# Optimization experiments

Hardware: AMD Instinct MI355X
Metric: run time of the kernel (lower is better)

The kernel has to match this reference:

```python
import jax, jax.numpy as jnp
import numpy as np

NUM_NODES = 256
IN_FEAT = 64
HIDDEN = 512
N_CLASSES = 2
BATCH = 256


def setup_inputs() -> dict:
    key = jax.random.key(0)
    ks = jax.random.split(key, 10)
    return {
        "z": jax.random.normal(ks[0], (BATCH, 1, NUM_NODES, NUM_NODES), dtype=jnp.float32),
        "node_emb": jax.random.normal(ks[1], (NUM_NODES, IN_FEAT), dtype=jnp.float32),
        "w1": jax.random.normal(ks[2], (IN_FEAT, HIDDEN), dtype=jnp.float32) * (1.0 / np.sqrt(IN_FEAT)),
        "b1": jnp.zeros((HIDDEN,), dtype=jnp.float32),
        "w2": jax.random.normal(ks[3], (HIDDEN, HIDDEN), dtype=jnp.float32) * (1.0 / np.sqrt(HIDDEN)),
        "b2": jnp.zeros((HIDDEN,), dtype=jnp.float32),
        "w3": jax.random.normal(ks[4], (HIDDEN, HIDDEN), dtype=jnp.float32) * (1.0 / np.sqrt(HIDDEN)),
        "b3": jnp.zeros((HIDDEN,), dtype=jnp.float32),
        "fcw": jax.random.normal(ks[5], (HIDDEN, N_CLASSES), dtype=jnp.float32) * (1.0 / np.sqrt(HIDDEN)),
        "fcb": jnp.zeros((N_CLASSES,), dtype=jnp.float32),
    }


def reference(z, node_emb, w1, b1, w2, b2, w3, b3, fcw, fcb):
    # z: (B, 1, N, N) latent interpreted as weighted adjacency
    z_sq = jnp.squeeze(z, axis=1)                         # (B, N, N)
    A = jax.nn.sigmoid(z_sq)
    A = (A + jnp.swapaxes(A, 1, 2)) * 0.5                  # symmetrize
    A_hat = A + jnp.eye(A.shape[-1], dtype=A.dtype)[None]  # add self loops
    D_hat = jnp.sum(A_hat, axis=2) + 1e-6                  # (B, N) degrees
    d_inv_sqrt = D_hat ** -0.5
    # norm_A = D^{-1/2} A_hat D^{-1/2} via row/col scaling (same math as diag bmm)
    norm_A = A_hat * d_inv_sqrt[:, :, None] * d_inv_sqrt[:, None, :]

    X = jnp.broadcast_to(node_emb[None], (z.shape[0],) + node_emb.shape)  # (B, N, F)
    H1 = jax.nn.relu(jnp.einsum('bij,bjh->bih', norm_A, X @ w1 + b1))
    H2 = jax.nn.relu(jnp.einsum('bij,bjh->bih', norm_A, H1 @ w2 + b2))
    H3 = jax.nn.relu(jnp.einsum('bij,bjh->bih', norm_A, H2 @ w3 + b3))
    graph_emb = jnp.mean(H3, axis=1)                       # (B, H)
    logits = graph_emb @ fcw + fcb                         # (B, n_classes)
    return logits
```

## Files before the change

### kernel.cpp

```cpp
#include <hip/hip_runtime.h>
#include <stdint.h>

#define B_ 256
#define N_ 256
#define F_ 64
#define H_ 512

typedef _Float16 f16;
typedef _Float16 f16x8 __attribute__((ext_vector_type(8)));
typedef _Float16 f16x4 __attribute__((ext_vector_type(4)));
typedef float    f32x4 __attribute__((ext_vector_type(4)));

__device__ __forceinline__ float sigmoidf_(float x) {
    return 1.0f / (1.0f + __expf(-x));
}

__global__ __launch_bounds__(256) void k_sums(const float* __restrict__ z,
                                              f16* __restrict__ S,
                                              float* __restrict__ R,
                                              float* __restrict__ Cpart) {
    int b = blockIdx.y, c = blockIdx.x;
    int tid = threadIdx.x, lane = tid & 63, w = tid >> 6;
    float colacc[4] = {0.f, 0.f, 0.f, 0.f};
    for (int r = 0; r < 16; r++) {
        int i = c * 64 + w * 16 + r;
        size_t base = ((size_t)(b * N_ + i)) * N_;
        float4 v = *(const float4*)(z + base + lane * 4);
        float s0 = sigmoidf_(v.x), s1 = sigmoidf_(v.y),
              s2 = sigmoidf_(v.z), s3 = sigmoidf_(v.w);
        f16x4 sv = { (f16)s0, (f16)s1, (f16)s2, (f16)s3 };
        *(f16x4*)(S + base + lane * 4) = sv;
        colacc[0] += s0; colacc[1] += s1; colacc[2] += s2; colacc[3] += s3;
        float rs = s0 + s1 + s2 + s3;
        for (int off = 32; off; off >>= 1) rs += __shfl_down(rs, off, 64);
        if (lane == 0) R[b * N_ + i] = rs;
    }
    __shared__ float cbuf[4][N_];
    #pragma unroll
    for (int k = 0; k < 4; k++) cbuf[w][lane * 4 + k] = colacc[k];
    __syncthreads();
    float s4 = cbuf[0][tid] + cbuf[1][tid] + cbuf[2][tid] + cbuf[3][tid];
    Cpart[((size_t)c * B_ + b) * N_ + tid] = s4;
}

__global__ __launch_bounds__(256) void k_norma3(const f16* __restrict__ S,
                                                const float* __restrict__ R,
                                                const float* __restrict__ Cpart,
                                                f16* __restrict__ nA) {
    __shared__ f16 T0[128 * 129];
    __shared__ f16 T1[128 * 129];
    __shared__ float Dv[N_];
    int b = blockIdx.y, t = blockIdx.x;
    int tid = threadIdx.x;
    const f16* Sb = S + (size_t)b * N_ * N_;
    f16* Ab = nA + (size_t)b * N_ * N_;

    float cs = Cpart[(size_t)b * N_ + tid]
             + Cpart[((size_t)B_ + b) * N_ + tid]
             + Cpart[((size_t)2 * B_ + b) * N_ + tid]
             + Cpart[((size_t)3 * B_ + b) * N_ + tid];
    Dv[tid] = rsqrtf(1.0f + 1e-6f + 0.5f * (R[b * N_ + tid] + cs));

    auto stage = [&](const f16* src, f16* dst) {
        #pragma unroll
        for (int it = 0; it < 8; it++) {
            int u = it * 256 + tid;
            int r = u >> 4, c8 = (u & 15) * 8;
            *(f16x8*)&dst[r * 129 + c8] = *(const f16x8*)&src[(size_t)r * N_ + c8];
        }
    };
    if (t == 0)      stage(Sb, T0);
    else if (t == 1) stage(Sb + 128 * N_ + 128, T0);
    else           { stage(Sb + 128, T0); stage(Sb + (size_t)128 * N_, T1); }
    __syncthreads();

    auto emit = [&](const f16* Dir, const f16* Mir, int i0, int j0) {
        #pragma unroll
        for (int it = 0; it < 8; it++) {
            int il = it * 16 + (tid >> 4), jl8 = (tid & 15) * 8;
            float di = Dv[i0 + il];
            f16x8 d = *(const f16x8*)&Dir[il * 129 + jl8];
            f16x8 o;
            #pragma unroll
            for (int k = 0; k < 8; k++) {
                float v = 0.5f * ((float)d[k] + (float)Mir[(jl8 + k) * 129 + il]);
                if (i0 + il == j0 + jl8 + k) v += 1.0f;
                o[k] = (f16)(v * di * Dv[j0 + jl8 + k]);
            }
            *(f16x8*)&Ab[(size_t)(i0 + il) * N_ + j0 + jl8] = o;
        }
    };
    if (t == 0)      emit(T0, T0, 0, 0);
    else if (t == 1) emit(T0, T0, 128, 128);
    else           { emit(T0, T1, 0, 128); emit(T1, T0, 128, 0); }
}

__global__ __launch_bounds__(256) void k_prep(const float* __restrict__ ne,
                                              const float* __restrict__ w1,
                                              const float* __restrict__ b1,
                                              const float* __restrict__ w2,
                                              const float* __restrict__ w3,
                                              f16* __restrict__ XW1t,
                                              f16* __restrict__ w2t,
                                              f16* __restrict__ w3t) {
    int bid = blockIdx.x;
    if (bid < 512) {
        int h = bid, node = threadIdx.x;
        float s = b1[h];
        #pragma unroll 8
        for (int k = 0; k < F_; k++) s += ne[node * F_ + k] * w1[k * H_ + h];
        XW1t[h * N_ + node] = (f16)s;
    } else {
        int idx4 = bid - 512;
        int which = idx4 >> 10;
        const float* src = which ? w3 : w2;
        f16* dst = which ? w3t : w2t;
        int idx = (idx4 & 1023) * 256 + threadIdx.x;
        int k = idx >> 9, n = idx & 511;
        dst[n * H_ + k] = (f16)src[k * H_ + n];
    }
}

template <int KDIM, int MODE>
__global__ __launch_bounds__(256, 4) void k_gemm(const f16* __restrict__ A, long aBatch,
                                                 const f16* __restrict__ Bt, long bBatch,
                                                 f16* __restrict__ Out,
                                                 const float* __restrict__ bias,
                                                 float* __restrict__ gp) {
    __shared__ f16 As[128 * 64];
    __shared__ f16 Bs[128 * 64];
    const int tid  = threadIdx.x;
    const int lane = tid & 63, wave = tid >> 6;
    const int wm = wave >> 1, wn = wave & 1;

    const int lin = blockIdx.x;
    const int xcd = lin & 7, q = lin >> 3;
    const int n_t = q & 3, p = q >> 2;
    const int grp = xcd * 64 + p;
    const int b   = grp >> 1, m_t = grp & 1;
    const int m0 = m_t * 128, n0 = n_t * 128;

    const f16* Ab = A + (size_t)b * aBatch;
    const f16* Bb = Bt + (size_t)b * bBatch;

    f32x4 acc[4][4];
    #pragma unroll
    for (int i = 0; i < 4; i++)
        #pragma unroll
        for (int j = 0; j < 4; j++)
            #pragma unroll
            for (int r = 0; r < 4; r++) acc[i][j][r] = 0.0f;

    const int lr = lane >> 3;
    const int kc = (lane & 7) ^ lr;

    const int ln15 = lane & 15;

    for (int kk = 0; kk < KDIM; kk += 64) {
        #pragma unroll
        for (int c = 0; c < 4; c++) {
            int chunk = wave * 4 + c;
            int row = chunk * 8 + lr;
            __builtin_amdgcn_global_load_lds(
                (__attribute__((address_space(1))) void*)(Ab + (size_t)(m0 + row) * KDIM + kk + kc * 8),
                (__attribute__((address_space(3))) void*)(&As[chunk * 512]), 16, 0, 0);
            __builtin_amdgcn_global_load_lds(
                (__attribute__((address_space(1))) void*)(Bb + (size_t)(n0 + row) * KDIM + kk + kc * 8),
                (__attribute__((address_space(3))) void*)(&Bs[chunk * 512]), 16, 0, 0);
        }
        __syncthreads();

        #pragma unroll
        for (int ks = 0; ks < 2; ks++) {
            const int rkc = ks * 4 + (lane >> 4);
            f16x8 aF[4];
            #pragma unroll
            for (int t = 0; t < 4; t++) {
                int ra = wm * 64 + t * 16 + ln15;
                aF[t] = *(const f16x8*)&As[(ra * 8 + (rkc ^ (ra & 7))) * 8];
            }
            #pragma unroll
            for (int h2 = 0; h2 < 2; h2++) {
                f16x8 bF[2];
                #pragma unroll
                for (int t = 0; t < 2; t++) {
                    int rb = wn * 64 + (h2 * 2 + t) * 16 + ln15;
                    bF[t] = *(const f16x8*)&Bs[(rb * 8 + (rkc ^ (rb & 7))) * 8];
                }
                #pragma unroll
                for (int mt = 0; mt < 4; mt++)
                    #pragma unroll
                    for (int t = 0; t < 2; t++)
                        acc[mt][h2 * 2 + t] = __builtin_amdgcn_mfma_f32_16x16x32_f16(aF[mt], bF[t], acc[mt][h2 * 2 + t], 0, 0, 0);
            }
        }
        __syncthreads();
    }

    const int quad = lane >> 4;
    if (MODE == 0) {
        f16* Ob = Out + (size_t)b * (N_ * H_);
        #pragma unroll
        for (int mt = 0; mt < 4; mt++) {
            int node = m0 + wm * 64 + mt * 16 + quad * 4;
            #pragma unroll
            for (int nt = 0; nt < 4; nt++) {
                int h = n0 + wn * 64 + nt * 16 + ln15;
                #pragma unroll
                for (int rr = 0; rr < 4; rr++) {
                    float v = acc[mt][nt][rr];
                    v = v > 0.f ? v : 0.f;
                    Ob[(size_t)(node + rr) * H_ + h] = (f16)v;
                }
            }
        }
    } else if (MODE == 1) {
        f16* Ob = Out + (size_t)b * (H_ * N_);
        #pragma unroll
        for (int nt = 0; nt < 4; nt++) {
            int n = n0 + wn * 64 + nt * 16 + ln15;
            float bv = bias[n];
            #pragma unroll
            for (int mt = 0; mt < 4; mt++) {
                int node = m0 + wm * 64 + mt * 16 + quad * 4;
                f16x4 v;
                #pragma unroll
                for (int rr = 0; rr < 4; rr++) v[rr] = (f16)(acc[mt][nt][rr] + bv);
                *(f16x4*)&Ob[(size_t)n * N_ + node] = v;
            }
        }
    } else {
        float part[4];
        #pragma unroll
        for (int nt = 0; nt < 4; nt++) {
            float partial = 0.f;
            #pragma unroll
            for (int mt = 0; mt < 4; mt++)
                #pragma unroll
                for (int rr = 0; rr < 4; rr++) {
                    float v = acc[mt][nt][rr];
                    partial += (v > 0.f ? v : 0.f);
                }
            partial += __shfl_down(partial, 32, 64);
            partial += __shfl_down(partial, 16, 64);
            part[nt] = partial;
        }
        __syncthreads();
        float* red = (float*)&As[0];
        if (quad == 0) {
            #pragma unroll
            for (int nt = 0; nt < 4; nt++)
                red[wave * 64 + nt * 16 + ln15] = part[nt];
        }
        __syncthreads();
        if (tid < 128) {
            int wnl = tid >> 6, hl = tid & 63;
            float v = red[wnl * 64 + hl] + red[(wnl + 2) * 64 + hl];
            gp[((size_t)m_t * B_ + b) * H_ + n0 + wnl * 64 + hl] = v;
        }
    }
}

__global__ __launch_bounds__(256) void k_logits(const float* __restrict__ gp,
                                                const float* __restrict__ fcw,
                                                const float* __restrict__ fcb,
                                                float* __restrict__ out) {
    int b = blockIdx.x, tid = threadIdx.x;
    const float* g0p = gp + (size_t)b * H_;
    const float* g1p = gp + (size_t)(B_ + b) * H_;
    float g0 = g0p[tid] + g1p[tid];
    float g1 = g0p[tid + 256] + g1p[tid + 256];
    float p0 = g0 * fcw[tid * 2 + 0] + g1 * fcw[(tid + 256) * 2 + 0];
    float p1 = g0 * fcw[tid * 2 + 1] + g1 * fcw[(tid + 256) * 2 + 1];
    for (int off = 32; off; off >>= 1) {
        p0 += __shfl_down(p0, off, 64);
        p1 += __shfl_down(p1, off, 64);
    }
    __shared__ float r0[4], r1[4];
    int lane = tid & 63, w = tid >> 6;
    if (lane == 0) { r0[w] = p0; r1[w] = p1; }
    __syncthreads();
    const float inv = 1.0f / N_;
    if (tid == 0) out[b * 2 + 0] = (r0[0] + r0[1] + r0[2] + r0[3]) * inv + fcb[0];
    if (tid == 1) out[b * 2 + 1] = (r1[0] + r1[1] + r1[2] + r1[3]) * inv + fcb[1];
}

extern "C" void kernel_launch(void* const* d_in, const int* in_sizes, int n_in,
                              void* d_out, int out_size, void* d_ws, size_t ws_size,
                              hipStream_t stream) {
    const float* z   = (const float*)d_in[0];
    const float* ne  = (const float*)d_in[1];
    const float* w1  = (const float*)d_in[2];
    const float* b1  = (const float*)d_in[3];
    const float* w2  = (const float*)d_in[4];
    const float* b2  = (const float*)d_in[5];
    const float* w3  = (const float*)d_in[6];
    const float* b3  = (const float*)d_in[7];
    const float* fcw = (const float*)d_in[8];
    const float* fcb = (const float*)d_in[9];
    float* out = (float*)d_out;

    char* ws = (char*)d_ws;
    f16*   T     = (f16*)(ws + 0);
    float* R     = (float*)(ws + 0);
    float* Cpart = (float*)(ws + 262144);
    f16*   nA    = (f16*)(ws + 67108864);
    f16*   Hh    = (f16*)(ws + 100663296);
    f16*   S     = (f16*)(ws + 100663296);
    float* gpart = (float*)(ws + 100663296);
    f16*   XW1t  = (f16*)(ws + 167772160);
    f16*   w2t   = (f16*)(ws + 168034304);
    f16*   w3t   = (f16*)(ws + 168558592);

    k_sums  <<<dim3(4, B_), 256, 0, stream>>>(z, S, R, Cpart);
    k_norma3<<<dim3(3, B_), 256, 0, stream>>>(S, R, Cpart, nA);
    k_prep  <<<2560,        256, 0, stream>>>(ne, w1, b1, w2, w3, XW1t, w2t, w3t);

    k_gemm<256, 0><<<2048, 256, 0, stream>>>(nA, 65536, XW1t, 0, Hh, nullptr, nullptr);
    k_gemm<512, 1><<<2048, 256, 0, stream>>>(Hh, 131072, w2t, 0, T, b2, nullptr);
    k_gemm<256, 0><<<2048, 256, 0, stream>>>(nA, 65536, T, 131072, Hh, nullptr, nullptr);
    k_gemm<512, 1><<<2048, 256, 0, stream>>>(Hh, 131072, w3t, 0, T, b3, nullptr);
    k_gemm<256, 2><<<2048, 256, 0, stream>>>(nA, 65536, T, 131072, nullptr, nullptr, gpart);

    k_logits<<<B_, 256, 0, stream>>>(gpart, fcw, fcb, out);
}
```

Measured before the change: 332.1 us.

## Load GEMM MFMA fragments directly from global memory and merge prep kernels

The batched GEMM no longer stages A and B tiles through LDS. Each wave now loads its MFMA fragments straight from global memory into registers, double-buffered with a ping-pong register scheme, which removes the LDS round trips and block-wide barriers. Launch bounds drop to 3 blocks per SM to make room for the extra registers. The sigmoid/sum kernel and the weight-prep kernel are merged into one launch to save a kernel launch. The risk is that each wave now fetches overlapping rows without LDS sharing, which raises global and L2 traffic, and that the lower occupancy hides latency less well.

After: 596.8 us. 1.8x slower.

```diff
diff --git a/kernel.cpp b/kernel.cpp
--- a/kernel.cpp
+++ b/kernel.cpp
@@ -15,32 +15,58 @@
     return 1.0f / (1.0f + __expf(-x));
 }
 
-__global__ __launch_bounds__(256) void k_sums(const float* __restrict__ z,
-                                              f16* __restrict__ S,
-                                              float* __restrict__ R,
-                                              float* __restrict__ Cpart) {
-    int b = blockIdx.y, c = blockIdx.x;
-    int tid = threadIdx.x, lane = tid & 63, w = tid >> 6;
-    float colacc[4] = {0.f, 0.f, 0.f, 0.f};
-    for (int r = 0; r < 16; r++) {
-        int i = c * 64 + w * 16 + r;
-        size_t base = ((size_t)(b * N_ + i)) * N_;
-        float4 v = *(const float4*)(z + base + lane * 4);
-        float s0 = sigmoidf_(v.x), s1 = sigmoidf_(v.y),
-              s2 = sigmoidf_(v.z), s3 = sigmoidf_(v.w);
-        f16x4 sv = { (f16)s0, (f16)s1, (f16)s2, (f16)s3 };
-        *(f16x4*)(S + base + lane * 4) = sv;
-        colacc[0] += s0; colacc[1] += s1; colacc[2] += s2; colacc[3] += s3;
-        float rs = s0 + s1 + s2 + s3;
-        for (int off = 32; off; off >>= 1) rs += __shfl_down(rs, off, 64);
-        if (lane == 0) R[b * N_ + i] = rs;
+__global__ __launch_bounds__(256) void k_pre(const float* __restrict__ z,
+                                             const float* __restrict__ ne,
+                                             const float* __restrict__ w1,
+                                             const float* __restrict__ b1,
+                                             const float* __restrict__ w2,
+                                             const float* __restrict__ w3,
+                                             f16* __restrict__ S,
+                                             float* __restrict__ R,
+                                             float* __restrict__ Cpart,
+                                             f16* __restrict__ XW1t,
+                                             f16* __restrict__ w2t,
+                                             f16* __restrict__ w3t) {
+    int bid = blockIdx.x;
+    int tid = threadIdx.x;
+    if (bid < 1024) {
+        int b = bid >> 2, c = bid & 3;
+        int lane = tid & 63, w = tid >> 6;
+        float colacc[4] = {0.f, 0.f, 0.f, 0.f};
+        for (int r = 0; r < 16; r++) {
+            int i = c * 64 + w * 16 + r;
+            size_t base = ((size_t)(b * N_ + i)) * N_;
+            float4 v = *(const float4*)(z + base + lane * 4);
+            float s0 = sigmoidf_(v.x), s1 = sigmoidf_(v.y),
+                  s2 = sigmoidf_(v.z), s3 = sigmoidf_(v.w);
+            f16x4 sv = { (f16)s0, (f16)s1, (f16)s2, (f16)s3 };
+            *(f16x4*)(S + base + lane * 4) = sv;
+            colacc[0] += s0; colacc[1] += s1; colacc[2] += s2; colacc[3] += s3;
+            float rs = s0 + s1 + s2 + s3;
+            for (int off = 32; off; off >>= 1) rs += __shfl_down(rs, off, 64);
+            if (lane == 0) R[b * N_ + i] = rs;
+        }
+        __shared__ float cbuf[4][N_];
+        #pragma unroll
+        for (int k = 0; k < 4; k++) cbuf[w][lane * 4 + k] = colacc[k];
+        __syncthreads();
+        float s4 = cbuf[0][tid] + cbuf[1][tid] + cbuf[2][tid] + cbuf[3][tid];
+        Cpart[((size_t)c * B_ + b) * N_ + tid] = s4;
+    } else if (bid < 1536) {
+        int h = bid - 1024, node = tid;
+        float s = b1[h];
+        #pragma unroll 8
+        for (int k = 0; k < F_; k++) s += ne[node * F_ + k] * w1[k * H_ + h];
+        XW1t[h * N_ + node] = (f16)s;
+    } else {
+        int idx4 = bid - 1536;
+        int which = idx4 >> 10;
+        const float* src = which ? w3 : w2;
+        f16* dst = which ? w3t : w2t;
+        int idx = (idx4 & 1023) * 256 + tid;
+        int k = idx >> 9, n = idx & 511;
+        dst[n * H_ + k] = (f16)src[k * H_ + n];
     }
-    __shared__ float cbuf[4][N_];
-    #pragma unroll
-    for (int k = 0; k < 4; k++) cbuf[w][lane * 4 + k] = colacc[k];
-    __syncthreads();
-    float s4 = cbuf[0][tid] + cbuf[1][tid] + cbuf[2][tid] + cbuf[3][tid];
-    Cpart[((size_t)c * B_ + b) * N_ + tid] = s4;
 }
 
 __global__ __launch_bounds__(256) void k_norma3(const f16* __restrict__ S,
@@ -95,43 +121,17 @@
     else           { emit(T0, T1, 0, 128); emit(T1, T0, 128, 0); }
 }
 
-__global__ __launch_bounds__(256) void k_prep(const float* __restrict__ ne,
-                                              const float* __restrict__ w1,
-                                              const float* __restrict__ b1,
-                                              const float* __restrict__ w2,
-                                              const float* __restrict__ w3,
-                                              f16* __restrict__ XW1t,
-                                              f16* __restrict__ w2t,
-                                              f16* __restrict__ w3t) {
-    int bid = blockIdx.x;
-    if (bid < 512) {
-        int h = bid, node = threadIdx.x;
-        float s = b1[h];
-        #pragma unroll 8
-        for (int k = 0; k < F_; k++) s += ne[node * F_ + k] * w1[k * H_ + h];
-        XW1t[h * N_ + node] = (f16)s;
-    } else {
-        int idx4 = bid - 512;
-        int which = idx4 >> 10;
-        const float* src = which ? w3 : w2;
-        f16* dst = which ? w3t : w2t;
-        int idx = (idx4 & 1023) * 256 + threadIdx.x;
-        int k = idx >> 9, n = idx & 511;
-        dst[n * H_ + k] = (f16)src[k * H_ + n];
-    }
-}
-
 template <int KDIM, int MODE>
-__global__ __launch_bounds__(256, 4) void k_gemm(const f16* __restrict__ A, long aBatch,
+__global__ __launch_bounds__(256, 3) void k_gemm(const f16* __restrict__ A, long aBatch,
                                                  const f16* __restrict__ Bt, long bBatch,
                                                  f16* __restrict__ Out,
                                                  const float* __restrict__ bias,
                                                  float* __restrict__ gp) {
-    __shared__ f16 As[128 * 64];
-    __shared__ f16 Bs[128 * 64];
+    __shared__ float red[256];
     const int tid  = threadIdx.x;
     const int lane = tid & 63, wave = tid >> 6;
     const int wm = wave >> 1, wn = wave & 1;
+    const int ln15 = lane & 15, rkc = lane >> 4;
 
     const int lin = blockIdx.x;
     const int xcd = lin & 7, q = lin >> 3;
@@ -140,9 +140,6 @@
     const int b   = grp >> 1, m_t = grp & 1;
     const int m0 = m_t * 128, n0 = n_t * 128;
 
-    const f16* Ab = A + (size_t)b * aBatch;
-    const f16* Bb = Bt + (size_t)b * bBatch;
-
     f32x4 acc[4][4];
     #pragma unroll
     for (int i = 0; i < 4; i++)
@@ -151,53 +148,37 @@
             #pragma unroll
             for (int r = 0; r < 4; r++) acc[i][j][r] = 0.0f;
 
-    const int lr = lane >> 3;
-    const int kc = (lane & 7) ^ lr;
-
-    const int ln15 = lane & 15;
-
-    for (int kk = 0; kk < KDIM; kk += 64) {
-        #pragma unroll
-        for (int c = 0; c < 4; c++) {
-            int chunk = wave * 4 + c;
-            int row = chunk * 8 + lr;
-            __builtin_amdgcn_global_load_lds(
-                (__attribute__((address_space(1))) void*)(Ab + (size_t)(m0 + row) * KDIM + kk + kc * 8),
-                (__attribute__((address_space(3))) void*)(&As[chunk * 512]), 16, 0, 0);
-            __builtin_amdgcn_global_load_lds(
-                (__attribute__((address_space(1))) void*)(Bb + (size_t)(n0 + row) * KDIM + kk + kc * 8),
-                (__attribute__((address_space(3))) void*)(&Bs[chunk * 512]), 16, 0, 0);
-        }
-        __syncthreads();
-
-        #pragma unroll
-        for (int ks = 0; ks < 2; ks++) {
-            const int rkc = ks * 4 + (lane >> 4);
-            f16x8 aF[4];
-            #pragma unroll
-            for (int t = 0; t < 4; t++) {
-                int ra = wm * 64 + t * 16 + ln15;
-                aF[t] = *(const f16x8*)&As[(ra * 8 + (rkc ^ (ra & 7))) * 8];
-            }
-            #pragma unroll
-            for (int h2 = 0; h2 < 2; h2++) {
-                f16x8 bF[2];
-                #pragma unroll
-                for (int t = 0; t < 2; t++) {
-                    int rb = wn * 64 + (h2 * 2 + t) * 16 + ln15;
-                    bF[t] = *(const f16x8*)&Bs[(rb * 8 + (rkc ^ (rb & 7))) * 8];
-                }
-                #pragma unroll
-                for (int mt = 0; mt < 4; mt++)
-                    #pragma unroll
-                    for (int t = 0; t < 2; t++)
-                        acc[mt][h2 * 2 + t] = __builtin_amdgcn_mfma_f32_16x16x32_f16(aF[mt], bF[t], acc[mt][h2 * 2 + t], 0, 0, 0);
-            }
-        }
-        __syncthreads();
+    const f16* pA = A  + (size_t)b * aBatch + (size_t)(m0 + wm * 64 + ln15) * KDIM + rkc * 8;
+    const f16* pB = Bt + (size_t)b * bBatch + (size_t)(n0 + wn * 64 + ln15) * KDIM + rkc * 8;
+
+    f16x8 aC[4], bC[4], aN[4], bN[4];
+
+    auto load4 = [&](f16x8* af, f16x8* bf, int s) {
+        #pragma unroll
+        for (int t = 0; t < 4; t++) {
+            af[t] = *(const f16x8*)(pA + (size_t)t * 16 * KDIM + s * 32);
+            bf[t] = *(const f16x8*)(pB + (size_t)t * 16 * KDIM + s * 32);
+        }
+    };
+    auto domfma = [&](const f16x8* af, const f16x8* bf) {
+        #pragma unroll
+        for (int mt = 0; mt < 4; mt++)
+            #pragma unroll
+            for (int nt = 0; nt < 4; nt++)
+                acc[mt][nt] = __builtin_amdgcn_mfma_f32_16x16x32_f16(af[mt], bf[nt], acc[mt][nt], 0, 0, 0);
+    };
+
+    constexpr int NS = KDIM / 32;
+    load4(aC, bC, 0);
+    #pragma unroll 1
+    for (int s = 0; s < NS; s += 2) {
+        load4(aN, bN, s + 1);
+        domfma(aC, bC);
+        if (s + 2 < NS) load4(aC, bC, s + 2);
+        domfma(aN, bN);
     }
 
-    const int quad = lane >> 4;
+    const int quad = rkc;
     if (MODE == 0) {
         f16* Ob = Out + (size_t)b * (N_ * H_);
         #pragma unroll
@@ -245,8 +226,6 @@
             partial += __shfl_down(partial, 16, 64);
             part[nt] = partial;
         }
-        __syncthreads();
-        float* red = (float*)&As[0];
         if (quad == 0) {
             #pragma unroll
             for (int nt = 0; nt < 4; nt++)
@@ -312,9 +291,8 @@
     f16*   w2t   = (f16*)(ws + 168034304);
     f16*   w3t   = (f16*)(ws + 168558592);
 
-    k_sums  <<<dim3(4, B_), 256, 0, stream>>>(z, S, R, Cpart);
+    k_pre   <<<3584,        256, 0, stream>>>(z, ne, w1, b1, w2, w3, S, R, Cpart, XW1t, w2t, w3t);
     k_norma3<<<dim3(3, B_), 256, 0, stream>>>(S, R, Cpart, nA);
-    k_prep  <<<2560,        256, 0, stream>>>(ne, w1, b1, w2, w3, XW1t, w2t, w3t);
 
     k_gemm<256, 0><<<2048, 256, 0, stream>>>(nA, 65536, XW1t, 0, Hh, nullptr, nullptr);
     k_gemm<512, 1><<<2048, 256, 0, stream>>>(Hh, 131072, w2t, 0, T, b2, nullptr);
```

## Merge sigmoid-sum and weight prep kernels, split rows finer, rotate GEMM K-order

Applied to the files above, without the earlier changes.

The sigmoid/row-column sum kernel and the weight preparation kernel become one launch with 4608 blocks. Each sum block now covers 32 rows instead of 64, so there are 8 column partials, and the normalisation kernel sums all 8. The GEMM K-loop start is rotated per block so concurrent blocks read different K slices, which is meant to spread memory and cache traffic. The cost is one fewer launch and more parallelism in the sum stage, in exchange for more partial-sum traffic and a less predictable access order.

New measurement: 335.4 us. No clear change (+1.0%).

```diff
diff --git a/kernel.cpp b/kernel.cpp
--- a/kernel.cpp
+++ b/kernel.cpp
@@ -15,32 +15,58 @@
     return 1.0f / (1.0f + __expf(-x));
 }
 
-__global__ __launch_bounds__(256) void k_sums(const float* __restrict__ z,
-                                              f16* __restrict__ S,
-                                              float* __restrict__ R,
-                                              float* __restrict__ Cpart) {
-    int b = blockIdx.y, c = blockIdx.x;
-    int tid = threadIdx.x, lane = tid & 63, w = tid >> 6;
-    float colacc[4] = {0.f, 0.f, 0.f, 0.f};
-    for (int r = 0; r < 16; r++) {
-        int i = c * 64 + w * 16 + r;
-        size_t base = ((size_t)(b * N_ + i)) * N_;
-        float4 v = *(const float4*)(z + base + lane * 4);
-        float s0 = sigmoidf_(v.x), s1 = sigmoidf_(v.y),
-              s2 = sigmoidf_(v.z), s3 = sigmoidf_(v.w);
-        f16x4 sv = { (f16)s0, (f16)s1, (f16)s2, (f16)s3 };
-        *(f16x4*)(S + base + lane * 4) = sv;
-        colacc[0] += s0; colacc[1] += s1; colacc[2] += s2; colacc[3] += s3;
-        float rs = s0 + s1 + s2 + s3;
-        for (int off = 32; off; off >>= 1) rs += __shfl_down(rs, off, 64);
-        if (lane == 0) R[b * N_ + i] = rs;
+__global__ __launch_bounds__(256) void k_pre(const float* __restrict__ z,
+                                             const float* __restrict__ ne,
+                                             const float* __restrict__ w1,
+                                             const float* __restrict__ b1,
+                                             const float* __restrict__ w2,
+                                             const float* __restrict__ w3,
+                                             f16* __restrict__ S,
+                                             float* __restrict__ R,
+                                             float* __restrict__ Cpart,
+                                             f16* __restrict__ XW1t,
+                                             f16* __restrict__ w2t,
+                                             f16* __restrict__ w3t) {
+    int bid = blockIdx.x;
+    int tid = threadIdx.x;
+    if (bid < 2048) {
+        int b = bid >> 3, c = bid & 7;
+        int lane = tid & 63, w = tid >> 6;
+        float colacc[4] = {0.f, 0.f, 0.f, 0.f};
+        for (int r = 0; r < 8; r++) {
+            int i = c * 32 + w * 8 + r;
+            size_t base = ((size_t)(b * N_ + i)) * N_;
+            float4 v = *(const float4*)(z + base + lane * 4);
+            float s0 = sigmoidf_(v.x), s1 = sigmoidf_(v.y),
+                  s2 = sigmoidf_(v.z), s3 = sigmoidf_(v.w);
+            f16x4 sv = { (f16)s0, (f16)s1, (f16)s2, (f16)s3 };
+            *(f16x4*)(S + base + lane * 4) = sv;
+            colacc[0] += s0; colacc[1] += s1; colacc[2] += s2; colacc[3] += s3;
+            float rs = s0 + s1 + s2 + s3;
+            for (int off = 32; off; off >>= 1) rs += __shfl_down(rs, off, 64);
+            if (lane == 0) R[b * N_ + i] = rs;
+        }
+        __shared__ float cbuf[4][N_];
+        #pragma unroll
+        for (int k = 0; k < 4; k++) cbuf[w][lane * 4 + k] = colacc[k];
+        __syncthreads();
+        float s4 = cbuf[0][tid] + cbuf[1][tid] + cbuf[2][tid] + cbuf[3][tid];
+        Cpart[((size_t)c * B_ + b) * N_ + tid] = s4;
+    } else if (bid < 2560) {
+        int h = bid - 2048, node = tid;
+        float s = b1[h];
+        #pragma unroll 8
+        for (int k = 0; k < F_; k++) s += ne[node * F_ + k] * w1[k * H_ + h];
+        XW1t[h * N_ + node] = (f16)s;
+    } else {
+        int idx4 = bid - 2560;
+        int which = idx4 >> 10;
+        const float* src = which ? w3 : w2;
+        f16* dst = which ? w3t : w2t;
+        int idx = (idx4 & 1023) * 256 + tid;
+        int k = idx >> 9, n = idx & 511;
+        dst[n * H_ + k] = (f16)src[k * H_ + n];
     }
-    __shared__ float cbuf[4][N_];
-    #pragma unroll
-    for (int k = 0; k < 4; k++) cbuf[w][lane * 4 + k] = colacc[k];
-    __syncthreads();
-    float s4 = cbuf[0][tid] + cbuf[1][tid] + cbuf[2][tid] + cbuf[3][tid];
-    Cpart[((size_t)c * B_ + b) * N_ + tid] = s4;
 }
 
 __global__ __launch_bounds__(256) void k_norma3(const f16* __restrict__ S,
@@ -55,10 +81,9 @@
     const f16* Sb = S + (size_t)b * N_ * N_;
     f16* Ab = nA + (size_t)b * N_ * N_;
 
-    float cs = Cpart[(size_t)b * N_ + tid]
-             + Cpart[((size_t)B_ + b) * N_ + tid]
-             + Cpart[((size_t)2 * B_ + b) * N_ + tid]
-             + Cpart[((size_t)3 * B_ + b) * N_ + tid];
+    float cs = 0.f;
+    #pragma unroll
+    for (int c = 0; c < 8; c++) cs += Cpart[((size_t)c * B_ + b) * N_ + tid];
     Dv[tid] = rsqrtf(1.0f + 1e-6f + 0.5f * (R[b * N_ + tid] + cs));
 
     auto stage = [&](const f16* src, f16* dst) {
@@ -93,32 +118,6 @@
     if (t == 0)      emit(T0, T0, 0, 0);
     else if (t == 1) emit(T0, T0, 128, 128);
     else           { emit(T0, T1, 0, 128); emit(T1, T0, 128, 0); }
-}
-
-__global__ __launch_bounds__(256) void k_prep(const float* __restrict__ ne,
-                                              const float* __restrict__ w1,
-                                              const float* __restrict__ b1,
-                                              const float* __restrict__ w2,
-                                              const float* __restrict__ w3,
-                                              f16* __restrict__ XW1t,
-                                              f16* __restrict__ w2t,
-                                              f16* __restrict__ w3t) {
-    int bid = blockIdx.x;
-    if (bid < 512) {
-        int h = bid, node = threadIdx.x;
-        float s = b1[h];
-        #pragma unroll 8
-        for (int k = 0; k < F_; k++) s += ne[node * F_ + k] * w1[k * H_ + h];
-        XW1t[h * N_ + node] = (f16)s;
-    } else {
-        int idx4 = bid - 512;
-        int which = idx4 >> 10;
-        const float* src = which ? w3 : w2;
-        f16* dst = which ? w3t : w2t;
-        int idx = (idx4 & 1023) * 256 + threadIdx.x;
-        int k = idx >> 9, n = idx & 511;
-        dst[n * H_ + k] = (f16)src[k * H_ + n];
-    }
 }
 
 template <int KDIM, int MODE>
@@ -156,7 +155,11 @@
 
     const int ln15 = lane & 15;
 
-    for (int kk = 0; kk < KDIM; kk += 64) {
+    constexpr int NS = KDIM / 64;
+    const int srot = ((q >> 5) + q) & (NS - 1);
+
+    for (int si = 0; si < NS; si++) {
+        const int kk = ((si + srot) & (NS - 1)) * 64;
         #pragma unroll
         for (int c = 0; c < 4; c++) {
             int chunk = wave * 4 + c;
@@ -312,9 +315,8 @@
     f16*   w2t   = (f16*)(ws + 168034304);
     f16*   w3t   = (f16*)(ws + 168558592);
 
-    k_sums  <<<dim3(4, B_), 256, 0, stream>>>(z, S, R, Cpart);
+    k_pre   <<<4608,        256, 0, stream>>>(z, ne, w1, b1, w2, w3, S, R, Cpart, XW1t, w2t, w3t);
     k_norma3<<<dim3(3, B_), 256, 0, stream>>>(S, R, Cpart, nA);
-    k_prep  <<<2560,        256, 0, stream>>>(ne, w1, b1, w2, w3, XW1t, w2t, w3t);
 
     k_gemm<256, 0><<<2048, 256, 0, stream>>>(nA, 65536, XW1t, 0, Hh, nullptr, nullptr);
     k_gemm<512, 1><<<2048, 256, 0, stream>>>(Hh, 131072, w2t, 0, T, b2, nullptr);
```
